# Optimization experiments

Measured on AMD Instinct MI355X. Metric: run time of the kernel, lower is better.

The kernel has to match this reference:

```python
import jax, jax.numpy as jnp
import numpy as np

EPOCHS = 200
DECAY_W = 1.0
CO_LAMBDA = 0.1
N, C = 262144, 256


def setup_inputs() -> dict:
    key = jax.random.key(0)
    k1, k2, k3 = jax.random.split(key, 3)
    y_1 = jax.random.normal(k1, (N, C), dtype=jnp.float32)
    y_2 = jax.random.normal(k2, (N, C), dtype=jnp.float32)
    t = jax.random.randint(k3, (N,), 0, C, dtype=jnp.int64)
    return {"y_1": y_1, "y_2": y_2, "t": t, "epoch": 50}


def reference(y_1, y_2, t, epoch):
    n, c = y_1.shape
    increment = 0.5 / EPOCHS

    logp1 = jax.nn.log_softmax(y_1, axis=1)
    logp2 = jax.nn.log_softmax(y_2, axis=1)
    # per-sample cross-entropy losses
    ce1 = -jnp.take_along_axis(logp1, t[:, None], axis=1)[:, 0]
    ce2 = -jnp.take_along_axis(logp2, t[:, None], axis=1)[:, 0]
    loss_pick = ce1 + ce2  # [N]

    # sample-selection: keep the num_remember smallest losses
    mean_v = jnp.mean(loss_pick)
    remember_rate_small = jnp.mean((loss_pick < mean_v).astype(jnp.float32))
    remember_rate = jnp.maximum(1.0 - increment * epoch, remember_rate_small)
    num_remember = jnp.floor(remember_rate * n).astype(jnp.int32)
    order = jnp.argsort(loss_pick)
    ranks = jnp.argsort(order)          # rank of each sample in ascending loss order
    remember = ranks < num_remember     # boolean mask == ind_update membership
    loss_clean = jnp.sum(jnp.where(remember, loss_pick, 0.0)) / n

    # ind_update_1 = {1..N-1} \\ ind_update  (original code excludes index 0)
    idx = jnp.arange(n)
    not_upd = jnp.logical_and(jnp.logical_not(remember), idx != 0)

    p1 = jnp.exp(logp1)
    p2 = jnp.exp(logp2)
    pred1 = jnp.argmax(y_1, axis=1)
    pred2 = jnp.argmax(y_2, axis=1)
    pmax1 = jnp.max(p1, axis=1)
    pmax2 = jnp.max(p2, axis=1)

    thresh = 1.0 - (1.0 - min(0.5, 1.0 / n)) * epoch / EPOCHS
    cond = (pred1 != t) & (pred1 == pred2) & (pmax1 * pmax2 > thresh)
    dc = not_upd & cond

    # pseudo-label CE with adaptive weight on the dc subset
    w = (pmax1 * pmax2) ** (0.5 - 0.5 * epoch / EPOCHS)
    ce_dc = (-jnp.take_along_axis(logp1, pred1[:, None], axis=1)[:, 0]
             - jnp.take_along_axis(logp2, pred1[:, None], axis=1)[:, 0])
    loss_dc = jnp.sum(jnp.where(dc, w * ce_dc, 0.0)) / n

    remain = not_upd & jnp.logical_not(cond)
    loss1 = jnp.sum(jnp.where(remain, loss_pick, 0.0)) / n

    # symmetric KL consistency (kl_loss_compute both directions, tempature=1)
    kl12 = jnp.mean(jnp.sum(p2 * (logp2 - logp1), axis=1))
    kl21 = jnp.mean(jnp.sum(p1 * (logp1 - logp2), axis=1))
    inter_view_loss = kl12 + kl21

    return loss_clean + loss_dc + DECAY_W * loss1 + CO_LAMBDA * inter_view_loss
```

## Files before the change

### kernel.cpp

```cpp
#include <hip/hip_runtime.h>
#include <hip/hip_bf16.h>
#include <math.h>

#define NROWS 262144
#define NCOLS 256
#define G1    2048
#define WT    (G1 * 4)
#define KST   (NROWS / 4 / WT)
#define G3    512
#define G7    1024
#define TIE_CAP 2048

struct Scal {
    double   sum_loss;
    double   sum_iv;
    float    mean_v;
    int      cnt_below;
    int      rank;
    int      sel_a;
    int      sel_b;
    unsigned tau_key;
    int      need;
    int      tie_cnt;
};

__device__ __forceinline__ unsigned f2key(float f) {
    unsigned u = __float_as_uint(f);
    return (u & 0x80000000u) ? ~u : (u | 0x80000000u);
}

template<int C>
__device__ __forceinline__ float dppf(float x) {
    return __int_as_float(__builtin_amdgcn_update_dpp(0, __float_as_int(x), C, 0xF, 0xF, true));
}
template<int C>
__device__ __forceinline__ int dppi(int x) {
    return __builtin_amdgcn_update_dpp(0, x, C, 0xF, 0xF, true);
}

__global__ void k_init(int* p, int n) {
    int i = blockIdx.x * blockDim.x + threadIdx.x;
    if (i < n) p[i] = 0;
}

__global__ void k_main(
    const float* __restrict__ y1, const float* __restrict__ y2,
    const int* __restrict__ t, const int* __restrict__ ep,
    float* __restrict__ loss, float* __restrict__ dcv,
    double* __restrict__ pb)
{
    const int lane = threadIdx.x & 63;
    const int wave = threadIdx.x >> 6;
    const int grp  = lane >> 4;
    const int gl   = lane & 15;
    const int gwave = blockIdx.x * (blockDim.x >> 6) + wave;

    const float fep    = (float)ep[0];
    const float expw   = 0.5f - 0.5f * fep / 200.0f;
    const float thresh = 1.0f - (1.0f - fminf(0.5f, 1.0f / (float)NROWS)) * fep / 200.0f;
    const float lthresh = __logf(thresh);

    double acc_loss = 0.0, acc_iv = 0.0;

#define AMAX_INIT(av, bv)                                            \
    m1 = (av).x; i1 = 4 * gl; bsel = (bv).x;                         \
    m2 = (bv).x; i2 = 4 * gl;                                        \
    {                                                                \
        const int ib = 4 * gl;                                       \
        if ((av).y > m1) { m1 = (av).y; i1 = ib + 1; bsel = (bv).y; }\
        if ((av).z > m1) { m1 = (av).z; i1 = ib + 2; bsel = (bv).z; }\
        if ((av).w > m1) { m1 = (av).w; i1 = ib + 3; bsel = (bv).w; }\
        if ((bv).y > m2) { m2 = (bv).y; i2 = ib + 1; }               \
        if ((bv).z > m2) { m2 = (bv).z; i2 = ib + 2; }               \
        if ((bv).w > m2) { m2 = (bv).w; i2 = ib + 3; }               \
    }

#define AMAX_CHUNK(av, bv, c)                                        \
    {                                                                \
        const int ib = (c) * 64 + 4 * gl;                            \
        if ((av).x > m1) { m1 = (av).x; i1 = ib;     bsel = (bv).x; }\
        if ((av).y > m1) { m1 = (av).y; i1 = ib + 1; bsel = (bv).y; }\
        if ((av).z > m1) { m1 = (av).z; i1 = ib + 2; bsel = (bv).z; }\
        if ((av).w > m1) { m1 = (av).w; i1 = ib + 3; bsel = (bv).w; }\
        if ((bv).x > m2) { m2 = (bv).x; i2 = ib; }                   \
        if ((bv).y > m2) { m2 = (bv).y; i2 = ib + 1; }               \
        if ((bv).z > m2) { m2 = (bv).z; i2 = ib + 2; }               \
        if ((bv).w > m2) { m2 = (bv).w; i2 = ib + 3; }               \
    }

#define ECC(av, bv)                                                           \
    {                                                                         \
        const float e10 = __expf((av).x), e11 = __expf((av).y);               \
        const float e12 = __expf((av).z), e13 = __expf((av).w);               \
        const float e20 = __expf((bv).x), e21 = __expf((bv).y);               \
        const float e22 = __expf((bv).z), e23 = __expf((bv).w);               \
        const float d0 = (av).x - (bv).x, d1 = (av).y - (bv).y;               \
        const float d2 = (av).z - (bv).z, d3 = (av).w - (bv).w;               \
        z1 += (e10 + e11) + (e12 + e13);                                      \
        z2 += (e20 + e21) + (e22 + e23);                                      \
        As += (e10 * d0 + e11 * d1) + (e12 * d2 + e13 * d3);                  \
        Bs -= (e20 * d0 + e21 * d1) + (e22 * d2 + e23 * d3);                  \
    }

    int row  = (gwave) * 4 + grp;
    int tc0  = t[row];
    int tc1  = t[row + WT * 4];
    int tc2  = 0;
    float y1t0 = y1[(size_t)row * NCOLS + tc0];
    float y2t0 = y2[(size_t)row * NCOLS + tc0];
    float y1t1 = 0.f, y2t1 = 0.f;

    float4 c0a, c1a, c0b, c1b, c2a, c3a, c2b, c3b;
    {
        const float4* __restrict__ q1 =
            reinterpret_cast<const float4*>(y1 + (size_t)row * NCOLS) + gl;
        const float4* __restrict__ q2 =
            reinterpret_cast<const float4*>(y2 + (size_t)row * NCOLS) + gl;
        c0a = q1[0]; c1a = q1[16]; c0b = q2[0]; c1b = q2[16];
    }

    #pragma unroll
    for (int k = 0; k < KST; k++) {
        const int rowN = row + WT * 4;
        const float4* __restrict__ q1 =
            reinterpret_cast<const float4*>(y1 + (size_t)row * NCOLS) + gl;
        const float4* __restrict__ q2 =
            reinterpret_cast<const float4*>(y2 + (size_t)row * NCOLS) + gl;

        c2a = q1[32]; c3a = q1[48]; c2b = q2[32]; c3b = q2[48];

        float m1, m2, bsel; int i1, i2;
        float z1 = 0.f, z2 = 0.f, As = 0.f, Bs = 0.f;
        AMAX_INIT(c0a, c0b)
        ECC(c0a, c0b)
        AMAX_CHUNK(c1a, c1b, 1)
        ECC(c1a, c1b)

        if (k < KST - 1) {
            const float4* __restrict__ n1 =
                reinterpret_cast<const float4*>(y1 + (size_t)rowN * NCOLS) + gl;
            const float4* __restrict__ n2 =
                reinterpret_cast<const float4*>(y2 + (size_t)rowN * NCOLS) + gl;
            c0a = n1[0]; c1a = n1[16]; c0b = n2[0]; c1b = n2[16];
            y1t1 = y1[(size_t)rowN * NCOLS + tc1];
            y2t1 = y2[(size_t)rowN * NCOLS + tc1];
        }
        if (k < KST - 2) tc2 = t[row + 2 * WT * 4];

        AMAX_CHUNK(c2a, c2b, 2)
        ECC(c2a, c2b)
        AMAX_CHUNK(c3a, c3b, 3)
        ECC(c3a, c3b)

#define RSTEP(C)                                                              \
        {                                                                     \
            const float rm1 = dppf<C>(m1); const int ri1 = dppi<C>(i1);       \
            const float rb  = dppf<C>(bsel);                                  \
            const float rm2 = dppf<C>(m2); const int ri2 = dppi<C>(i2);       \
            z1 += dppf<C>(z1); z2 += dppf<C>(z2);                             \
            As += dppf<C>(As); Bs += dppf<C>(Bs);                             \
            if (rm1 > m1 || (rm1 == m1 && ri1 < i1)) { m1 = rm1; i1 = ri1; bsel = rb; } \
            if (rm2 > m2 || (rm2 == m2 && ri2 < i2)) { m2 = rm2; i2 = ri2; }  \
        }
        RSTEP(0xB1)
        RSTEP(0x4E)
        RSTEP(0x124)
        RSTEP(0x128)
#undef RSTEP

        const float y2p = bsel;

        const float lz1 = __logf(z1), lz2 = __logf(z2);
        const float lp  = (lz1 - y1t0) + (lz2 - y2t0);
        const float ppx = (m1 + m2) - (lz1 + lz2);
        const bool cond = (i1 != tc0) && (i1 == i2) && (ppx > lthresh);
        const float wgt = __expf(expw * ppx);
        const float cedc = (lz1 - m1) + (lz2 - y2p);
        const float dv = cond ? fmaxf(wgt * cedc, 0.0f) : -1.0f;
        const float iv = As * __builtin_amdgcn_rcpf(z1)
                       + Bs * __builtin_amdgcn_rcpf(z2);

        if (gl == 0) {
            loss[row] = lp;
            dcv[row]  = dv;
            acc_loss += (double)lp;
            acc_iv   += (double)iv;
        }

        row = rowN; tc0 = tc1; tc1 = tc2; y1t0 = y1t1; y2t0 = y2t1;
    }

#undef ECC
#undef AMAX_CHUNK
#undef AMAX_INIT

    __shared__ double sl[16], si[16];
    if (gl == 0) { sl[wave * 4 + grp] = acc_loss; si[wave * 4 + grp] = acc_iv; }
    __syncthreads();
    if (threadIdx.x == 0) {
        double a = 0.0, b = 0.0;
        #pragma unroll
        for (int i = 0; i < 16; i++) { a += sl[i]; b += si[i]; }
        pb[blockIdx.x * 2 + 0] = a;
        pb[blockIdx.x * 2 + 1] = b;
    }
}

__global__ void k_reduce_pb(const double* __restrict__ pb, Scal* sc) {
    __shared__ double s1[256], s2[256];
    int th = threadIdx.x;
    double a = 0.0, b = 0.0;
    for (int i = th; i < G1; i += 256) { a += pb[i * 2]; b += pb[i * 2 + 1]; }
    s1[th] = a; s2[th] = b; __syncthreads();
    for (int off = 128; off; off >>= 1) {
        if (th < off) { s1[th] += s1[th + off]; s2[th] += s2[th + off]; }
        __syncthreads();
    }
    if (th == 0) {
        sc->sum_loss = s1[0];
        sc->sum_iv   = s2[0];
        sc->mean_v   = (float)(s1[0] / (double)NROWS);
    }
}

__global__ __launch_bounds__(256) void k_histA(const float* __restrict__ loss,
                                               Scal* sc, int* __restrict__ histA) {
    __shared__ int lh[2048];
    __shared__ int cbel;
    int th = threadIdx.x;
    for (int i = th; i < 2048; i += 256) lh[i] = 0;
    if (th == 0) cbel = 0;
    __syncthreads();
    const float mv = sc->mean_v;
    int stride = G3 * 256;
    for (int i = blockIdx.x * 256 + th; i < NROWS; i += stride) {
        float v = loss[i];
        unsigned long long m = __ballot(v < mv);
        if ((th & 63) == 0) atomicAdd(&cbel, __popcll(m));
        atomicAdd(&lh[f2key(v) >> 21], 1);
    }
    __syncthreads();
    if (th == 0 && cbel) atomicAdd(&sc->cnt_below, cbel);
    for (int i = th; i < 2048; i += 256) {
        int v = lh[i];
        if (v) atomicAdd(&histA[i], v);
    }
}

__global__ __launch_bounds__(256) void k_histB(const float* __restrict__ loss,
                                               const Scal* __restrict__ sc,
                                               int* __restrict__ histB) {
    __shared__ int lh[2048];
    int th = threadIdx.x;
    for (int i = th; i < 2048; i += 256) lh[i] = 0;
    __syncthreads();
    const unsigned a = (unsigned)sc->sel_a;
    int stride = G3 * 256;
    for (int i = blockIdx.x * 256 + th; i < NROWS; i += stride) {
        unsigned key = f2key(loss[i]);
        if ((key >> 21) == a) atomicAdd(&lh[(key >> 10) & 0x7FFu], 1);
    }
    __syncthreads();
    for (int i = th; i < 2048; i += 256) {
        int v = lh[i];
        if (v) atomicAdd(&histB[i], v);
    }
}

__global__ __launch_bounds__(256) void k_histC(const float* __restrict__ loss,
                                               const Scal* __restrict__ sc,
                                               int* __restrict__ histC) {
    __shared__ int lh[1024];
    int th = threadIdx.x;
    for (int i = th; i < 1024; i += 256) lh[i] = 0;
    __syncthreads();
    const unsigned ab = ((unsigned)sc->sel_a << 11) | (unsigned)sc->sel_b;
    int stride = G3 * 256;
    for (int i = blockIdx.x * 256 + th; i < NROWS; i += stride) {
        unsigned key = f2key(loss[i]);
        if ((key >> 10) == ab) atomicAdd(&lh[key & 0x3FFu], 1);
    }
    __syncthreads();
    for (int i = th; i < 1024; i += 256) {
        int v = lh[i];
        if (v) atomicAdd(&histC[i], v);
    }
}

__global__ void k_select(const int* __restrict__ hist, Scal* sc,
                         const int* __restrict__ ep, int nbins, int stage) {
    __shared__ int part[256];
    __shared__ int pref[256];
    __shared__ int rank_sh;
    int th = threadIdx.x;
    int bpt = nbins >> 8;
    if (th == 0) {
        int r;
        if (stage == 0) {
            float rrs = (float)sc->cnt_below / (float)NROWS;
            float rr = fmaxf(1.0f - 0.0025f * (float)ep[0], rrs);
            int k = (int)floorf(rr * (float)NROWS);
            if (k < 1) k = 1;
            if (k > NROWS) k = NROWS;
            r = k;
        } else {
            r = sc->rank;
        }
        rank_sh = r;
    }
    __syncthreads();
    int s = 0;
    for (int b = 0; b < bpt; b++) s += hist[th * bpt + b];
    part[th] = s;
    __syncthreads();
    if (th == 0) { int c = 0; for (int i = 0; i < 256; i++) { pref[i] = c; c += part[i]; } }
    __syncthreads();
    int r = rank_sh;
    if (pref[th] < r && r <= pref[th] + part[th]) {
        int c = pref[th];
        for (int b = 0; b < bpt; b++) {
            int h = hist[th * bpt + b];
            if (c + h >= r) {
                int bin = th * bpt + b;
                if (stage == 0)      { sc->sel_a = bin; sc->rank = r - c; }
                else if (stage == 1) { sc->sel_b = bin; sc->rank = r - c; }
                else {
                    sc->tau_key = ((unsigned)sc->sel_a << 21) |
                                  ((unsigned)sc->sel_b << 10) | (unsigned)bin;
                    sc->need = r - c;
                }
                break;
            }
            c += h;
        }
    }
}

__global__ __launch_bounds__(256) void k_classify(
    const float* __restrict__ loss, const float* __restrict__ dcv,
    Scal* sc, int* __restrict__ tiebuf, double* __restrict__ pc)
{
    __shared__ double s0[256], s1v[256], s2v[256];
    int th = threadIdx.x;
    unsigned tk = sc->tau_key;
    double cl = 0.0, cd = 0.0, c1 = 0.0;
    for (int i = blockIdx.x * blockDim.x + th; i < NROWS; i += blockDim.x * gridDim.x) {
        float lp = loss[i];
        unsigned key = f2key(lp);
        if (key < tk) {
            cl += (double)lp;
        } else if (key > tk) {
            if (i != 0) {
                float d = dcv[i];
                if (d >= 0.0f) cd += (double)d;
                else           c1 += (double)lp;
            }
        } else {
            int slot = atomicAdd(&sc->tie_cnt, 1);
            if (slot < TIE_CAP) tiebuf[slot] = i;
        }
    }
    s0[th] = cl; s1v[th] = cd; s2v[th] = c1;
    __syncthreads();
    for (int off = 128; off; off >>= 1) {
        if (th < off) { s0[th] += s0[th + off]; s1v[th] += s1v[th + off]; s2v[th] += s2v[th + off]; }
        __syncthreads();
    }
    if (th == 0) {
        pc[blockIdx.x * 3 + 0] = s0[0];
        pc[blockIdx.x * 3 + 1] = s1v[0];
        pc[blockIdx.x * 3 + 2] = s2v[0];
    }
}

__global__ void k_final(const double* __restrict__ pc,
                        const float* __restrict__ loss, const float* __restrict__ dcv,
                        Scal* sc, int* __restrict__ tiebuf, float* __restrict__ out)
{
    __shared__ double s0[256], s1v[256], s2v[256];
    int th = threadIdx.x;
    double a = 0.0, b = 0.0, c = 0.0;
    for (int i = th; i < G7; i += 256) { a += pc[i * 3]; b += pc[i * 3 + 1]; c += pc[i * 3 + 2]; }
    s0[th] = a; s1v[th] = b; s2v[th] = c;
    __syncthreads();
    for (int off = 128; off; off >>= 1) {
        if (th < off) { s0[th] += s0[th + off]; s1v[th] += s1v[th + off]; s2v[th] += s2v[th + off]; }
        __syncthreads();
    }
    if (th == 0) {
        double sum_clean = s0[0], sum_dc = s1v[0], sum_1 = s2v[0];
        int nt = sc->tie_cnt;
        if (nt > TIE_CAP) nt = TIE_CAP;
        for (int i = 1; i < nt; i++) {
            int v = tiebuf[i]; int j = i - 1;
            while (j >= 0 && tiebuf[j] > v) { tiebuf[j + 1] = tiebuf[j]; j--; }
            tiebuf[j + 1] = v;
        }
        int need = sc->need;
        for (int s = 0; s < nt; s++) {
            int idx = tiebuf[s];
            float lp = loss[idx];
            if (s < need) {
                sum_clean += (double)lp;
            } else if (idx != 0) {
                float d = dcv[idx];
                if (d >= 0.0f) sum_dc += (double)d;
                else           sum_1 += (double)lp;
            }
        }
        double invN = 1.0 / (double)NROWS;
        out[0] = (float)((sum_clean + sum_dc + sum_1) * invN + 0.1 * sc->sum_iv * invN);
    }
}

extern "C" void kernel_launch(void* const* d_in, const int* in_sizes, int n_in,
                              void* d_out, int out_size, void* d_ws, size_t ws_size,
                              hipStream_t stream) {
    const float* y1 = (const float*)d_in[0];
    const float* y2 = (const float*)d_in[1];
    const int*   t  = (const int*)d_in[2];
    const int*   ep = (const int*)d_in[3];
    float* out = (float*)d_out;

    char* w = (char*)d_ws;
    Scal*   sc     = (Scal*)w;
    int*    histA  = (int*)(w + 256);
    int*    histB  = (int*)(w + 256 + 8192);
    int*    histC  = (int*)(w + 256 + 16384);
    float*  loss   = (float*)(w + 256 + 20480);
    float*  dcv    = (float*)(w + 256 + 20480 + NROWS * 4);
    double* pb     = (double*)(w + 256 + 20480 + NROWS * 8);
    double* pc     = (double*)(w + 256 + 20480 + NROWS * 8 + G1 * 16);
    int*    tiebuf = (int*)(w + 256 + 20480 + NROWS * 8 + G1 * 16 + G7 * 24);

    const int nzero = (256 + 20480) / 4;
    k_init<<<(nzero + 255) / 256, 256, 0, stream>>>((int*)d_ws, nzero);

    k_main<<<G1, 256, 0, stream>>>(y1, y2, t, ep, loss, dcv, pb);
    k_reduce_pb<<<1, 256, 0, stream>>>(pb, sc);
    k_histA<<<G3, 256, 0, stream>>>(loss, sc, histA);
    k_select<<<1, 256, 0, stream>>>(histA, sc, ep, 2048, 0);
    k_histB<<<G3, 256, 0, stream>>>(loss, sc, histB);
    k_select<<<1, 256, 0, stream>>>(histB, sc, ep, 2048, 1);
    k_histC<<<G3, 256, 0, stream>>>(loss, sc, histC);
    k_select<<<1, 256, 0, stream>>>(histC, sc, ep, 1024, 2);
    k_classify<<<G7, 256, 0, stream>>>(loss, dcv, sc, tiebuf, pc);
    k_final<<<1, 256, 0, stream>>>(pc, loss, dcv, sc, tiebuf, out);
}
```

Baseline: 156.4 us.

## Replace persistent software-pipelined row loop with one row per group launch

The main kernel previously ran a fixed grid of 2048 blocks, with each 16-lane group looping over 8 rows and prefetching the next row's data while computing the current one. It now launches 16384 blocks, each group handles a single row, and all loads are issued up front. This removes the manual pipelining and the per-thread loop state, relying on more resident waves to hide memory latency. The cost is eight times as many per-block partial sums for the downstream reduction, plus more block launch and sync overhead.

```diff
diff --git a/kernel.cpp b/kernel.cpp
--- a/kernel.cpp
+++ b/kernel.cpp
@@ -4,9 +4,7 @@
 
 #define NROWS 262144
 #define NCOLS 256
-#define G1    2048
-#define WT    (G1 * 4)
-#define KST   (NROWS / 4 / WT)
+#define G1    16384
 #define G3    512
 #define G7    1024
 #define TIE_CAP 2048
@@ -53,28 +51,38 @@
     const int wave = threadIdx.x >> 6;
     const int grp  = lane >> 4;
     const int gl   = lane & 15;
-    const int gwave = blockIdx.x * (blockDim.x >> 6) + wave;
+    const int row  = blockIdx.x * 16 + wave * 4 + grp;
 
     const float fep    = (float)ep[0];
     const float expw   = 0.5f - 0.5f * fep / 200.0f;
     const float thresh = 1.0f - (1.0f - fminf(0.5f, 1.0f / (float)NROWS)) * fep / 200.0f;
     const float lthresh = __logf(thresh);
 
-    double acc_loss = 0.0, acc_iv = 0.0;
-
-#define AMAX_INIT(av, bv)                                            \
-    m1 = (av).x; i1 = 4 * gl; bsel = (bv).x;                         \
-    m2 = (bv).x; i2 = 4 * gl;                                        \
-    {                                                                \
-        const int ib = 4 * gl;                                       \
-        if ((av).y > m1) { m1 = (av).y; i1 = ib + 1; bsel = (bv).y; }\
-        if ((av).z > m1) { m1 = (av).z; i1 = ib + 2; bsel = (bv).z; }\
-        if ((av).w > m1) { m1 = (av).w; i1 = ib + 3; bsel = (bv).w; }\
-        if ((bv).y > m2) { m2 = (bv).y; i2 = ib + 1; }               \
-        if ((bv).z > m2) { m2 = (bv).z; i2 = ib + 2; }               \
-        if ((bv).w > m2) { m2 = (bv).w; i2 = ib + 3; }               \
-    }
-
+    const int tc = t[row];
+
+    const float4* __restrict__ q1 =
+        reinterpret_cast<const float4*>(y1 + (size_t)row * NCOLS) + gl;
+    const float4* __restrict__ q2 =
+        reinterpret_cast<const float4*>(y2 + (size_t)row * NCOLS) + gl;
+
+    const float4 c0a = q1[0],  c1a = q1[16], c2a = q1[32], c3a = q1[48];
+    const float4 c0b = q2[0],  c1b = q2[16], c2b = q2[32], c3b = q2[48];
+
+    const float y1t = y1[(size_t)row * NCOLS + tc];
+    const float y2t = y2[(size_t)row * NCOLS + tc];
+
+    float m1, m2, bsel; int i1, i2;
+    m1 = c0a.x; i1 = 4 * gl; bsel = c0b.x;
+    m2 = c0b.x; i2 = 4 * gl;
+    {
+        const int ib = 4 * gl;
+        if (c0a.y > m1) { m1 = c0a.y; i1 = ib + 1; bsel = c0b.y; }
+        if (c0a.z > m1) { m1 = c0a.z; i1 = ib + 2; bsel = c0b.z; }
+        if (c0a.w > m1) { m1 = c0a.w; i1 = ib + 3; bsel = c0b.w; }
+        if (c0b.y > m2) { m2 = c0b.y; i2 = ib + 1; }
+        if (c0b.z > m2) { m2 = c0b.z; i2 = ib + 2; }
+        if (c0b.w > m2) { m2 = c0b.w; i2 = ib + 3; }
+    }
 #define AMAX_CHUNK(av, bv, c)                                        \
     {                                                                \
         const int ib = (c) * 64 + 4 * gl;                            \
@@ -87,7 +95,12 @@
         if ((bv).z > m2) { m2 = (bv).z; i2 = ib + 2; }               \
         if ((bv).w > m2) { m2 = (bv).w; i2 = ib + 3; }               \
     }
-
+    AMAX_CHUNK(c1a, c1b, 1)
+    AMAX_CHUNK(c2a, c2b, 2)
+    AMAX_CHUNK(c3a, c3b, 3)
+#undef AMAX_CHUNK
+
+    float z1 = 0.f, z2 = 0.f, As = 0.f, Bs = 0.f;
 #define ECC(av, bv)                                                           \
     {                                                                         \
         const float e10 = __expf((av).x), e11 = __expf((av).y);               \
@@ -101,101 +114,47 @@
         As += (e10 * d0 + e11 * d1) + (e12 * d2 + e13 * d3);                  \
         Bs -= (e20 * d0 + e21 * d1) + (e22 * d2 + e23 * d3);                  \
     }
-
-    int row  = (gwave) * 4 + grp;
-    int tc0  = t[row];
-    int tc1  = t[row + WT * 4];
-    int tc2  = 0;
-    float y1t0 = y1[(size_t)row * NCOLS + tc0];
-    float y2t0 = y2[(size_t)row * NCOLS + tc0];
-    float y1t1 = 0.f, y2t1 = 0.f;
-
-    float4 c0a, c1a, c0b, c1b, c2a, c3a, c2b, c3b;
-    {
-        const float4* __restrict__ q1 =
-            reinterpret_cast<const float4*>(y1 + (size_t)row * NCOLS) + gl;
-        const float4* __restrict__ q2 =
-            reinterpret_cast<const float4*>(y2 + (size_t)row * NCOLS) + gl;
-        c0a = q1[0]; c1a = q1[16]; c0b = q2[0]; c1b = q2[16];
-    }
-
-    #pragma unroll
-    for (int k = 0; k < KST; k++) {
-        const int rowN = row + WT * 4;
-        const float4* __restrict__ q1 =
-            reinterpret_cast<const float4*>(y1 + (size_t)row * NCOLS) + gl;
-        const float4* __restrict__ q2 =
-            reinterpret_cast<const float4*>(y2 + (size_t)row * NCOLS) + gl;
-
-        c2a = q1[32]; c3a = q1[48]; c2b = q2[32]; c3b = q2[48];
-
-        float m1, m2, bsel; int i1, i2;
-        float z1 = 0.f, z2 = 0.f, As = 0.f, Bs = 0.f;
-        AMAX_INIT(c0a, c0b)
-        ECC(c0a, c0b)
-        AMAX_CHUNK(c1a, c1b, 1)
-        ECC(c1a, c1b)
-
-        if (k < KST - 1) {
-            const float4* __restrict__ n1 =
-                reinterpret_cast<const float4*>(y1 + (size_t)rowN * NCOLS) + gl;
-            const float4* __restrict__ n2 =
-                reinterpret_cast<const float4*>(y2 + (size_t)rowN * NCOLS) + gl;
-            c0a = n1[0]; c1a = n1[16]; c0b = n2[0]; c1b = n2[16];
-            y1t1 = y1[(size_t)rowN * NCOLS + tc1];
-            y2t1 = y2[(size_t)rowN * NCOLS + tc1];
-        }
-        if (k < KST - 2) tc2 = t[row + 2 * WT * 4];
-
-        AMAX_CHUNK(c2a, c2b, 2)
-        ECC(c2a, c2b)
-        AMAX_CHUNK(c3a, c3b, 3)
-        ECC(c3a, c3b)
+    ECC(c0a, c0b)
+    ECC(c1a, c1b)
+    ECC(c2a, c2b)
+    ECC(c3a, c3b)
+#undef ECC
 
 #define RSTEP(C)                                                              \
-        {                                                                     \
-            const float rm1 = dppf<C>(m1); const int ri1 = dppi<C>(i1);       \
-            const float rb  = dppf<C>(bsel);                                  \
-            const float rm2 = dppf<C>(m2); const int ri2 = dppi<C>(i2);       \
-            z1 += dppf<C>(z1); z2 += dppf<C>(z2);                             \
-            As += dppf<C>(As); Bs += dppf<C>(Bs);                             \
-            if (rm1 > m1 || (rm1 == m1 && ri1 < i1)) { m1 = rm1; i1 = ri1; bsel = rb; } \
-            if (rm2 > m2 || (rm2 == m2 && ri2 < i2)) { m2 = rm2; i2 = ri2; }  \
-        }
-        RSTEP(0xB1)
-        RSTEP(0x4E)
-        RSTEP(0x124)
-        RSTEP(0x128)
+    {                                                                         \
+        const float rm1 = dppf<C>(m1); const int ri1 = dppi<C>(i1);           \
+        const float rb  = dppf<C>(bsel);                                      \
+        const float rm2 = dppf<C>(m2); const int ri2 = dppi<C>(i2);           \
+        z1 += dppf<C>(z1); z2 += dppf<C>(z2);                                 \
+        As += dppf<C>(As); Bs += dppf<C>(Bs);                                 \
+        if (rm1 > m1 || (rm1 == m1 && ri1 < i1)) { m1 = rm1; i1 = ri1; bsel = rb; } \
+        if (rm2 > m2 || (rm2 == m2 && ri2 < i2)) { m2 = rm2; i2 = ri2; }      \
+    }
+    RSTEP(0xB1)
+    RSTEP(0x4E)
+    RSTEP(0x124)
+    RSTEP(0x128)
 #undef RSTEP
 
-        const float y2p = bsel;
-
-        const float lz1 = __logf(z1), lz2 = __logf(z2);
-        const float lp  = (lz1 - y1t0) + (lz2 - y2t0);
-        const float ppx = (m1 + m2) - (lz1 + lz2);
-        const bool cond = (i1 != tc0) && (i1 == i2) && (ppx > lthresh);
-        const float wgt = __expf(expw * ppx);
-        const float cedc = (lz1 - m1) + (lz2 - y2p);
-        const float dv = cond ? fmaxf(wgt * cedc, 0.0f) : -1.0f;
-        const float iv = As * __builtin_amdgcn_rcpf(z1)
-                       + Bs * __builtin_amdgcn_rcpf(z2);
-
-        if (gl == 0) {
-            loss[row] = lp;
-            dcv[row]  = dv;
-            acc_loss += (double)lp;
-            acc_iv   += (double)iv;
-        }
-
-        row = rowN; tc0 = tc1; tc1 = tc2; y1t0 = y1t1; y2t0 = y2t1;
-    }
-
-#undef ECC
-#undef AMAX_CHUNK
-#undef AMAX_INIT
+    const float y2p = bsel;
+
+    const float lz1 = __logf(z1), lz2 = __logf(z2);
+    const float lp  = (lz1 - y1t) + (lz2 - y2t);
+    const float ppx = (m1 + m2) - (lz1 + lz2);
+    const bool cond = (i1 != tc) && (i1 == i2) && (ppx > lthresh);
+    const float wgt = __expf(expw * ppx);
+    const float cedc = (lz1 - m1) + (lz2 - y2p);
+    const float dv = cond ? fmaxf(wgt * cedc, 0.0f) : -1.0f;
+    const float iv = As * __builtin_amdgcn_rcpf(z1)
+                   + Bs * __builtin_amdgcn_rcpf(z2);
 
     __shared__ double sl[16], si[16];
-    if (gl == 0) { sl[wave * 4 + grp] = acc_loss; si[wave * 4 + grp] = acc_iv; }
+    if (gl == 0) {
+        loss[row] = lp;
+        dcv[row]  = dv;
+        sl[wave * 4 + grp] = (double)lp;
+        si[wave * 4 + grp] = (double)iv;
+    }
     __syncthreads();
     if (threadIdx.x == 0) {
         double a = 0.0, b = 0.0;
```

Measured after the change: 168.5 us. 7.7% more time.
